# Kernel tuning notes

Hardware: AMD Instinct MI355X
Metric: run time of the kernel (lower is better)

Reference implementation:

```python
import jax, jax.numpy as jnp
import numpy as np

EPS = 1e-5
GN_GROUPS_DIV = 4  # nn.GroupNorm(out_ch // 4, out_ch)


def conv1x1(x, w, b=None):
    # x [B,C,H,W], w [O,C]
    y = jnp.einsum('bchw,oc->bohw', x, w)
    return y if b is None else y + b[None, :, None, None]


def conv2d(x, w, pad):
    return jax.lax.conv_general_dilated(
        x, w, (1, 1), [(pad, pad), (pad, pad)],
        dimension_numbers=('NCHW', 'OIHW', 'NCHW'))


def batchnorm(x, gamma, beta):
    # training-mode BatchNorm2d: batch statistics over (B,H,W)
    mu = jnp.mean(x, axis=(0, 2, 3), keepdims=True)
    var = jnp.var(x, axis=(0, 2, 3), keepdims=True)
    xn = (x - mu) * jax.lax.rsqrt(var + EPS)
    return xn * gamma[None, :, None, None] + beta[None, :, None, None]


def groupnorm(x, gamma, beta, groups):
    B, C, H, W = x.shape
    xg = x.reshape(B, groups, C // groups, H, W)
    mu = jnp.mean(xg, axis=(2, 3, 4), keepdims=True)
    var = jnp.var(xg, axis=(2, 3, 4), keepdims=True)
    xn = ((xg - mu) * jax.lax.rsqrt(var + EPS)).reshape(B, C, H, W)
    return xn * gamma[None, :, None, None] + beta[None, :, None, None]


def bilinear_sample(img, ys, xs):
    # Faithful to DSC._bilinear_interpolate_3D: floor/floor+1 coords are
    # clamped BEFORE computing weights, so samples exactly at the last
    # row/col get all-zero weights (output zeroed there), as in torch.
    H, W = img.shape[2], img.shape[3]
    y0 = jnp.floor(ys)
    x0 = jnp.floor(xs)
    y0c = jnp.clip(y0, 0, H - 1).astype(jnp.int32)
    y1c = jnp.clip(y0 + 1, 0, H - 1).astype(jnp.int32)
    x0c = jnp.clip(x0, 0, W - 1).astype(jnp.int32)
    x1c = jnp.clip(x0 + 1, 0, W - 1).astype(jnp.int32)
    y0f, y1f = y0c.astype(ys.dtype), y1c.astype(ys.dtype)
    x0f, x1f = x0c.astype(xs.dtype), x1c.astype(xs.dtype)
    w00 = (y1f - ys) * (x1f - xs)
    w01 = (y1f - ys) * (xs - x0f)
    w10 = (ys - y0f) * (x1f - xs)
    w11 = (ys - y0f) * (xs - x0f)
    g = lambda yy, xx: img[:, :, yy, xx]  # irregular gather, [B,C,H,W]
    return (g(y0c, x0c) * w00 + g(y0c, x1c) * w01 +
            g(y1c, x0c) * w10 + g(y1c, x1c) * w11)


def _forward(x, ca_w1, ca_w2, sa_w, gate_w, off_w, off_b, off_gamma, off_beta,
             dsc_w, dsc_b, gn_gamma, gn_beta, bn_gamma, bn_beta, prelu_a,
             out_w, out_b):
    B, C, H, W = x.shape
    res = x

    # --- ChannelAttention2D (CBAM): shared MLP on avg & max pooled desc ---
    avg = jnp.mean(x, axis=(2, 3), keepdims=True)          # [B,C,1,1]
    mx = jnp.max(x, axis=(2, 3), keepdims=True)
    mlp = lambda v: conv1x1(jax.nn.relu(conv1x1(v, ca_w1)), ca_w2)
    ca = jax.nn.sigmoid(mlp(avg) + mlp(mx))
    x_ca = x * ca

    # --- SpatialAttention2D (CBAM): 7x7 conv over [mean,max] channel maps ---
    s_avg = jnp.mean(x, axis=1, keepdims=True)
    s_max = jnp.max(x, axis=1, keepdims=True)
    sa = jax.nn.sigmoid(conv2d(jnp.concatenate([s_avg, s_max], axis=1), sa_w, pad=3))
    x_sa = x * sa

    # --- gate fuse ---
    fuse = x_sa + x_ca
    guide = jax.nn.sigmoid(conv1x1(fuse, gate_w))
    xg = x * guide

    # --- DSConv(kernel_size=1, morph=0, if_offset=True) ---
    # offset branch (computed as in torch; with num_points=1 the iterative
    # offset accumulation zeroes the center point, so offsets do NOT move
    # the sampling grid -> zero gradient flows to the offset conv)
    off = jnp.tanh(batchnorm(conv2d(xg, off_w, pad=1) + off_b[None, :, None, None],
                             off_gamma, off_beta))
    del off  # dead in fwd math for kernel_size=1 (faithful to source)

    ii = jnp.arange(H, dtype=x.dtype)[:, None] * jnp.ones((1, W), x.dtype)
    jj = jnp.ones((H, 1), x.dtype) * jnp.arange(W, dtype=x.dtype)[None, :]
    deformed = bilinear_sample(xg, ii, jj)  # identity gather except last row/col zeroed

    d = conv1x1(deformed, dsc_w, dsc_b)     # dsc_conv_x with (k,1)=(1,1) kernel
    d = groupnorm(d, gn_gamma, gn_beta, C // GN_GROUPS_DIV)
    d = jax.nn.relu(d)

    # --- residual + BN + PReLU + 1x1 out conv ---
    y = d + res
    y = batchnorm(y, bn_gamma, bn_beta)
    a = prelu_a.reshape(())
    y = jnp.where(y >= 0, y, a * y)
    return conv1x1(y, out_w, out_b)         # [B,1,H,W]


def setup_inputs() -> dict:
    key = jax.random.key(0)
    ks = jax.random.split(key, 12)
    B, C, H, W = 8, 64, 256, 256
    r = C // 16  # CBAM ratio 16
    f32 = jnp.float32
    n = lambda k, shp, s: (jax.random.normal(k, shp, dtype=f32) * s)
    return {
        'x': n(ks[0], (B, C, H, W), 1.0),
        'ca_w1': n(ks[1], (r, C), 0.1),
        'ca_w2': n(ks[2], (C, r), 0.1),
        'sa_w': n(ks[3], (1, 2, 7, 7), 0.1),
        'gate_w': n(ks[4], (C, C), 0.05),
        'off_w': n(ks[5], (2, C, 3, 3), 0.05),
        'off_b': jnp.zeros((2,), f32),
        'off_gamma': jnp.ones((2,), f32),
        'off_beta': jnp.zeros((2,), f32),
        'dsc_w': n(ks[6], (C, C), 0.05),
        'dsc_b': jnp.zeros((C,), f32),
        'gn_gamma': jnp.ones((C,), f32),
        'gn_beta': jnp.zeros((C,), f32),
        'bn_gamma': jnp.ones((C,), f32),
        'bn_beta': jnp.zeros((C,), f32),
        'prelu_a': jnp.full((1,), 0.25, f32),
        'out_w': n(ks[7], (1, C), 0.1),
        'out_b': jnp.zeros((1,), f32),
    }


def reference(x, ca_w1, ca_w2, sa_w, gate_w, off_w, off_b, off_gamma, off_beta,
              dsc_w, dsc_b, gn_gamma, gn_beta, bn_gamma, bn_beta, prelu_a,
              out_w, out_b):
    return _forward(x, ca_w1, ca_w2, sa_w, gate_w, off_w, off_b, off_gamma,
                    off_beta, dsc_w, dsc_b, gn_gamma, gn_beta, bn_gamma,
                    bn_beta, prelu_a, out_w, out_b)
```

## Files before the change

kernel.cpp:

```cpp
#include <hip/hip_runtime.h>

#define HW 65536
#define CB 64
#define NB 8

typedef __attribute__((ext_vector_type(4))) float f32x4;
typedef __attribute__((ext_vector_type(8))) short s16x8;

__device__ __forceinline__ float sigm(float v) { return 1.f / (1.f + __expf(-v)); }

__device__ __forceinline__ unsigned encf(float f) {
    unsigned u = __float_as_uint(f);
    return (u & 0x80000000u) ? ~u : (u | 0x80000000u);
}
__device__ __forceinline__ float decf(unsigned u) {
    return (u & 0x80000000u) ? __uint_as_float(u & 0x7fffffffu) : __uint_as_float(~u);
}
__device__ __forceinline__ unsigned f2bf(float f) {
    unsigned u = __float_as_uint(f);
    u += 0x7fffu + ((u >> 16) & 1u);
    return u >> 16;
}
__device__ __forceinline__ float bf2f(unsigned h) {
    return __uint_as_float(h << 16);
}
__device__ __forceinline__ int swz(int row, int w) { return (row << 5) + (w ^ ((row & 7) << 2)); }

__global__ __launch_bounds__(256) void k_stats(
    const float* __restrict__ x, float* __restrict__ pool_sum,
    unsigned* __restrict__ pool_max, float* __restrict__ s_avg,
    float* __restrict__ s_max)
{
    const int t = threadIdx.x;
    const int b = blockIdx.x >> 6;
    const int pbase = (blockIdx.x & 63) << 10;
    const int lane = t & 63, wave = t >> 6;
    __shared__ float csum[4][CB];
    __shared__ float cmax[4][CB];

    float ps0 = 0, ps1 = 0, ps2 = 0, ps3 = 0;
    float pm0 = -1e30f, pm1 = -1e30f, pm2 = -1e30f, pm3 = -1e30f;
    const size_t base = (size_t)b * CB * HW + pbase + 4 * t;
    for (int c = 0; c < CB; ++c) {
        const float4 v = *(const float4*)(x + base + (size_t)c * HW);
        ps0 += v.x; ps1 += v.y; ps2 += v.z; ps3 += v.w;
        pm0 = fmaxf(pm0, v.x); pm1 = fmaxf(pm1, v.y);
        pm2 = fmaxf(pm2, v.z); pm3 = fmaxf(pm3, v.w);
        float cs = v.x + v.y + v.z + v.w;
        float cm = fmaxf(fmaxf(v.x, v.y), fmaxf(v.z, v.w));
        #pragma unroll
        for (int off = 32; off; off >>= 1) {
            cs += __shfl_xor(cs, off);
            cm = fmaxf(cm, __shfl_xor(cm, off));
        }
        if (lane == 0) { csum[wave][c] = cs; cmax[wave][c] = cm; }
    }
    __syncthreads();
    if (t < CB) {
        const float s = csum[0][t] + csum[1][t] + csum[2][t] + csum[3][t];
        const float m = fmaxf(fmaxf(cmax[0][t], cmax[1][t]), fmaxf(cmax[2][t], cmax[3][t]));
        atomicAdd(&pool_sum[b * CB + t], s);
        atomicMax(&pool_max[b * CB + t], encf(m));
    }
    const float inv = 1.f / 64.f;
    float4 sa4 = {ps0 * inv, ps1 * inv, ps2 * inv, ps3 * inv};
    float4 sm4 = {pm0, pm1, pm2, pm3};
    *(float4*)(s_avg + (size_t)b * HW + pbase + 4 * t) = sa4;
    *(float4*)(s_max + (size_t)b * HW + pbase + 4 * t) = sm4;
}

__global__ __launch_bounds__(64) void k_ca(
    const float* __restrict__ pool_sum, const unsigned* __restrict__ pool_max,
    const float* __restrict__ w1, const float* __restrict__ w2,
    float* __restrict__ ca)
{
    __shared__ float av[CB], mv[CB], hh[8];
    const int b = blockIdx.x, t = threadIdx.x;
    av[t] = pool_sum[b * CB + t] * (1.f / (float)HW);
    mv[t] = decf(pool_max[b * CB + t]);
    __syncthreads();
    if (t < 8) {
        const int h = t & 3;
        const float* v = (t < 4) ? av : mv;
        float s = 0;
        for (int c = 0; c < CB; ++c) s += w1[h * CB + c] * v[c];
        hh[t] = fmaxf(s, 0.f);
    }
    __syncthreads();
    float s = 0;
    #pragma unroll
    for (int h = 0; h < 4; ++h) s += w2[t * 4 + h] * (hh[h] + hh[4 + h]);
    ca[b * CB + t] = sigm(s);
}

__global__ __launch_bounds__(256) void k_saconv(
    const float* __restrict__ s_avg, const float* __restrict__ s_max,
    const float* __restrict__ w, float* __restrict__ sa)
{
    const int b = blockIdx.x >> 8;
    const int pix = ((blockIdx.x & 255) << 8) | threadIdx.x;
    const int i = pix >> 8, j = pix & 255;
    float acc = 0.f;
    #pragma unroll
    for (int cin = 0; cin < 2; ++cin) {
        const float* src = (cin ? s_max : s_avg) + (size_t)b * HW;
        const float* wk = w + cin * 49;
        #pragma unroll
        for (int ki = 0; ki < 7; ++ki) {
            const int y = i + ki - 3;
            if ((unsigned)y < 256u) {
                #pragma unroll
                for (int kj = 0; kj < 7; ++kj) {
                    const int xx = j + kj - 3;
                    if ((unsigned)xx < 256u) acc += src[(y << 8) | xx] * wk[ki * 7 + kj];
                }
            }
        }
    }
    sa[(size_t)b * HW + pix] = sigm(acc);
}

__global__ __launch_bounds__(256, 3) void k_main(
    const float* __restrict__ x, const float* __restrict__ sa,
    const float* __restrict__ ca, const float* __restrict__ gw,
    const float* __restrict__ dw, const float* __restrict__ db,
    unsigned short* __restrict__ dbuf, float* __restrict__ gn_sum,
    float* __restrict__ gn_sq)
{
    __shared__ unsigned lds[12320];
    const int t = threadIdx.x;
    const int wv = t >> 6, l = t & 63, hi = l >> 4, lo = l & 15;
    const int b = blockIdx.x >> 9;
    const int pbase = (blockIdx.x & 511) << 7;

    {
        const int orow = t >> 2, cq = (t & 3) << 4;
        const float* gsrc = gw + (orow << 6) + cq;
        const float* dsrc = dw + (orow << 6) + cq;
        unsigned ug[8], ud[8];
        #pragma unroll
        for (int j = 0; j < 8; ++j) {
            ug[j] = f2bf(gsrc[2 * j]) | (f2bf(gsrc[2 * j + 1]) << 16);
            ud[j] = f2bf(dsrc[2 * j]) | (f2bf(dsrc[2 * j + 1]) << 16);
        }
        const int wbase = (t & 3) << 3;
        *(uint4*)&lds[swz(orow, wbase)]            = make_uint4(ug[0], ug[1], ug[2], ug[3]);
        *(uint4*)&lds[swz(orow, wbase + 4)]        = make_uint4(ug[4], ug[5], ug[6], ug[7]);
        *(uint4*)&lds[2048 + swz(orow, wbase)]     = make_uint4(ud[0], ud[1], ud[2], ud[3]);
        *(uint4*)&lds[2048 + swz(orow, wbase + 4)] = make_uint4(ud[4], ud[5], ud[6], ud[7]);
    }

    {
        const int px0 = l << 1;
        const float2 sv = *(const float2*)(sa + (size_t)b * HW + pbase + px0);
        unsigned ux0[8], ux1[8], uf0[8], uf1[8];
        #pragma unroll
        for (int j2 = 0; j2 < 8; ++j2) {
            const int c0 = (wv << 4) + 2 * j2;
            const float cv0 = ca[(b << 6) + c0];
            const float cv1 = ca[(b << 6) + c0 + 1];
            const float2 v0 = *(const float2*)(x + ((size_t)((b << 6) + c0)) * HW + pbase + px0);
            const float2 v1 = *(const float2*)(x + ((size_t)((b << 6) + c0 + 1)) * HW + pbase + px0);
            ux0[j2] = f2bf(v0.x) | (f2bf(v1.x) << 16);
            ux1[j2] = f2bf(v0.y) | (f2bf(v1.y) << 16);
            uf0[j2] = f2bf(v0.x * (sv.x + cv0)) | (f2bf(v1.x * (sv.x + cv1)) << 16);
            uf1[j2] = f2bf(v0.y * (sv.y + cv0)) | (f2bf(v1.y * (sv.y + cv1)) << 16);
        }
        const int wb = wv << 3;
        *(uint4*)&lds[8192 + swz(px0, wb)]         = make_uint4(ux0[0], ux0[1], ux0[2], ux0[3]);
        *(uint4*)&lds[8192 + swz(px0, wb + 4)]     = make_uint4(ux0[4], ux0[5], ux0[6], ux0[7]);
        *(uint4*)&lds[8192 + swz(px0 + 1, wb)]     = make_uint4(ux1[0], ux1[1], ux1[2], ux1[3]);
        *(uint4*)&lds[8192 + swz(px0 + 1, wb + 4)] = make_uint4(ux1[4], ux1[5], ux1[6], ux1[7]);
        *(uint4*)&lds[4096 + swz(px0, wb)]         = make_uint4(uf0[0], uf0[1], uf0[2], uf0[3]);
        *(uint4*)&lds[4096 + swz(px0, wb + 4)]     = make_uint4(uf0[4], uf0[5], uf0[6], uf0[7]);
        *(uint4*)&lds[4096 + swz(px0 + 1, wb)]     = make_uint4(uf1[0], uf1[1], uf1[2], uf1[3]);
        *(uint4*)&lds[4096 + swz(px0 + 1, wb + 4)] = make_uint4(uf1[4], uf1[5], uf1[6], uf1[7]);
    }
    __syncthreads();

    f32x4 acc[8];
    #pragma unroll
    for (int n = 0; n < 8; ++n) acc[n] = (f32x4){0.f, 0.f, 0.f, 0.f};
    {
        const int arow = (wv << 4) + lo;
        const s16x8 a0 = __builtin_bit_cast(s16x8, *(const uint4*)&lds[swz(arow, hi << 2)]);
        const s16x8 a1 = __builtin_bit_cast(s16x8, *(const uint4*)&lds[swz(arow, (hi << 2) + 16)]);
        #pragma unroll
        for (int n = 0; n < 8; ++n) {
            const int brow = (n << 4) + lo;
            const s16x8 b0 = __builtin_bit_cast(s16x8, *(const uint4*)&lds[4096 + swz(brow, hi << 2)]);
            const s16x8 b1 = __builtin_bit_cast(s16x8, *(const uint4*)&lds[4096 + swz(brow, (hi << 2) + 16)]);
            acc[n] = __builtin_amdgcn_mfma_f32_16x16x32_bf16(a0, b0, acc[n], 0, 0, 0);
            acc[n] = __builtin_amdgcn_mfma_f32_16x16x32_bf16(a1, b1, acc[n], 0, 0, 0);
        }
    }
    __syncthreads();

    {
        const bool row255 = (pbase >> 8) == 255;
        const bool halfblk = (pbase & 128) != 0;
        const int wb2 = (wv << 3) + (hi << 1);
        #pragma unroll
        for (int n = 0; n < 8; ++n) {
            const int pxl = (n << 4) + lo;
            const uint2 xv = *(const uint2*)&lds[8192 + swz(pxl, wb2)];
            const bool zero = row255 || (halfblk && pxl == 127);
            float xg0 = zero ? 0.f : bf2f(xv.x & 0xffffu) * sigm(acc[n][0]);
            float xg1 = zero ? 0.f : bf2f(xv.x >> 16)     * sigm(acc[n][1]);
            float xg2 = zero ? 0.f : bf2f(xv.y & 0xffffu) * sigm(acc[n][2]);
            float xg3 = zero ? 0.f : bf2f(xv.y >> 16)     * sigm(acc[n][3]);
            uint2 o;
            o.x = f2bf(xg0) | (f2bf(xg1) << 16);
            o.y = f2bf(xg2) | (f2bf(xg3) << 16);
            *(uint2*)&lds[4096 + swz(pxl, wb2)] = o;
        }
    }
    __syncthreads();

    f32x4 acc2[8];
    #pragma unroll
    for (int n = 0; n < 8; ++n) acc2[n] = (f32x4){0.f, 0.f, 0.f, 0.f};
    {
        const int arow = (wv << 4) + lo;
        const s16x8 a0 = __builtin_bit_cast(s16x8, *(const uint4*)&lds[2048 + swz(arow, hi << 2)]);
        const s16x8 a1 = __builtin_bit_cast(s16x8, *(const uint4*)&lds[2048 + swz(arow, (hi << 2) + 16)]);
        #pragma unroll
        for (int n = 0; n < 8; ++n) {
            const int brow = (n << 4) + lo;
            const s16x8 b0 = __builtin_bit_cast(s16x8, *(const uint4*)&lds[4096 + swz(brow, hi << 2)]);
            const s16x8 b1 = __builtin_bit_cast(s16x8, *(const uint4*)&lds[4096 + swz(brow, (hi << 2) + 16)]);
            acc2[n] = __builtin_amdgcn_mfma_f32_16x16x32_bf16(a0, b0, acc2[n], 0, 0, 0);
            acc2[n] = __builtin_amdgcn_mfma_f32_16x16x32_bf16(a1, b1, acc2[n], 0, 0, 0);
        }
    }

    float gs = 0.f, gq = 0.f;
    {
        const float4 bv = *(const float4*)(db + (wv << 4) + (hi << 2));
        const float bvr[4] = {bv.x, bv.y, bv.z, bv.w};
        unsigned short* lds16 = (unsigned short*)lds;
        #pragma unroll
        for (int n = 0; n < 8; ++n) {
            const int pxl = (n << 4) + lo;
            #pragma unroll
            for (int r = 0; r < 4; ++r) {
                const float dvf = acc2[n][r] + bvr[r];
                gs += dvf; gq += dvf * dvf;
                const int ch = (wv << 4) + (hi << 2) + r;
                const int w64 = (pxl >> 1) ^ ((ch & 7) << 2);
                lds16[((8192 + (ch << 6) + w64) << 1) + (pxl & 1)] = (unsigned short)f2bf(dvf);
            }
        }
    }
    #pragma unroll
    for (int o = 1; o < 16; o <<= 1) { gs += __shfl_xor(gs, o); gq += __shfl_xor(gq, o); }
    float* smf = (float*)&lds[12288];
    if (lo == 0) { smf[(((wv << 2) + hi) << 1)] = gs; smf[(((wv << 2) + hi) << 1) + 1] = gq; }
    __syncthreads();
    if (t < 16) {
        atomicAdd(&gn_sum[(b << 4) + t], smf[2 * t]);
        atomicAdd(&gn_sq[(b << 4) + t],  smf[2 * t + 1]);
    }
    {
        const int ch = t >> 2, sub = t & 3;
        unsigned short* dst = dbuf + ((size_t)((b << 6) + ch)) * HW + pbase;
        #pragma unroll
        for (int j = 0; j < 4; ++j) {
            const int w64 = ((j << 4) + (sub << 2)) ^ ((ch & 7) << 2);
            const uint4 dv = *(const uint4*)&lds[8192 + (ch << 6) + w64];
            *(uint4*)(dst + (j << 5) + (sub << 3)) = dv;
        }
    }
}

__global__ void k_fin_gn(const float* __restrict__ gn_sum, const float* __restrict__ gn_sq,
                         const float* __restrict__ gamma, const float* __restrict__ beta,
                         float* __restrict__ gn_a, float* __restrict__ gn_b)
{
    const int t = threadIdx.x;
    const int b = t >> 6, c = t & 63, g = c >> 2;
    const float n = 4.f * (float)HW;
    const float mu = gn_sum[b * 16 + g] / n;
    const float var = gn_sq[b * 16 + g] / n - mu * mu;
    const float a = rsqrtf(var + 1e-5f) * gamma[c];
    gn_a[t] = a;
    gn_b[t] = beta[c] - mu * a;
}

__global__ __launch_bounds__(256) void k_gnbn(
    const float* __restrict__ x, unsigned short* __restrict__ dy,
    const float* __restrict__ gn_a, const float* __restrict__ gn_b,
    float* __restrict__ bn_sum, float* __restrict__ bn_sq)
{
    const int t = threadIdx.x;
    const int bc = blockIdx.x >> 2;
    const int q = blockIdx.x & 3;
    const int c = bc & 63;
    const float a = gn_a[bc], bb = gn_b[bc];
    const size_t base0 = (size_t)bc * HW + ((size_t)q << 14);
    float bs = 0.f, bq = 0.f;
    for (int i = 0; i < 16; ++i) {
        const size_t base = base0 + (i << 10) + (t << 2);
        const ushort4 d4 = *(const ushort4*)(dy + base);
        const float4 xv = *(const float4*)(x + base);
        const float y0 = fmaxf(bf2f(d4.x) * a + bb, 0.f) + xv.x;
        const float y1 = fmaxf(bf2f(d4.y) * a + bb, 0.f) + xv.y;
        const float y2 = fmaxf(bf2f(d4.z) * a + bb, 0.f) + xv.z;
        const float y3 = fmaxf(bf2f(d4.w) * a + bb, 0.f) + xv.w;
        ushort4 o;
        o.x = (unsigned short)f2bf(y0); o.y = (unsigned short)f2bf(y1);
        o.z = (unsigned short)f2bf(y2); o.w = (unsigned short)f2bf(y3);
        *(ushort4*)(dy + base) = o;
        bs += y0 + y1 + y2 + y3;
        bq += y0 * y0 + y1 * y1 + y2 * y2 + y3 * y3;
    }
    #pragma unroll
    for (int off = 32; off; off >>= 1) { bs += __shfl_xor(bs, off); bq += __shfl_xor(bq, off); }
    __shared__ float rs[4], rq[4];
    if ((t & 63) == 0) { rs[t >> 6] = bs; rq[t >> 6] = bq; }
    __syncthreads();
    if (t == 0) {
        atomicAdd(&bn_sum[c], rs[0] + rs[1] + rs[2] + rs[3]);
        atomicAdd(&bn_sq[c],  rq[0] + rq[1] + rq[2] + rq[3]);
    }
}

__global__ void k_fin_bn(const float* __restrict__ bn_sum, const float* __restrict__ bn_sq,
                         const float* __restrict__ gamma, const float* __restrict__ beta,
                         float* __restrict__ bn_a, float* __restrict__ bn_b)
{
    const int c = threadIdx.x;
    const float n = (float)(NB * (size_t)HW);
    const float mu = bn_sum[c] / n;
    const float var = bn_sq[c] / n - mu * mu;
    const float a = rsqrtf(var + 1e-5f) * gamma[c];
    bn_a[c] = a;
    bn_b[c] = beta[c] - mu * a;
}

__global__ __launch_bounds__(256) void k_out(
    const unsigned short* __restrict__ y, const float* __restrict__ bn_a,
    const float* __restrict__ bn_b, const float* __restrict__ pa,
    const float* __restrict__ ow, const float* __restrict__ ob,
    float* __restrict__ out)
{
    const int t = threadIdx.x;
    const int b = blockIdx.x >> 6;
    const int p = ((blockIdx.x & 63) << 10) + (t << 2);
    const float alpha = pa[0];
    const float obv = ob[0];
    float a0 = obv, a1 = obv, a2 = obv, a3 = obv;
    for (int c = 0; c < CB; ++c) {
        const ushort4 v = *(const ushort4*)(y + ((size_t)(b * CB + c)) * HW + p);
        const float s = bn_a[c], sh = bn_b[c], w = ow[c];
        float t0 = bf2f(v.x) * s + sh; t0 = t0 >= 0.f ? t0 : alpha * t0; a0 += w * t0;
        float t1 = bf2f(v.y) * s + sh; t1 = t1 >= 0.f ? t1 : alpha * t1; a1 += w * t1;
        float t2 = bf2f(v.z) * s + sh; t2 = t2 >= 0.f ? t2 : alpha * t2; a2 += w * t2;
        float t3 = bf2f(v.w) * s + sh; t3 = t3 >= 0.f ? t3 : alpha * t3; a3 += w * t3;
    }
    float4 o = {a0, a1, a2, a3};
    *(float4*)(out + (size_t)b * HW + p) = o;
}

extern "C" void kernel_launch(void* const* d_in, const int* in_sizes, int n_in,
                              void* d_out, int out_size, void* d_ws, size_t ws_size,
                              hipStream_t stream)
{
    const float* x        = (const float*)d_in[0];
    const float* ca_w1    = (const float*)d_in[1];
    const float* ca_w2    = (const float*)d_in[2];
    const float* sa_w     = (const float*)d_in[3];
    const float* gate_w   = (const float*)d_in[4];
    const float* dsc_w    = (const float*)d_in[9];
    const float* dsc_b    = (const float*)d_in[10];
    const float* gn_gamma = (const float*)d_in[11];
    const float* gn_beta  = (const float*)d_in[12];
    const float* bn_gamma = (const float*)d_in[13];
    const float* bn_beta  = (const float*)d_in[14];
    const float* prelu_a  = (const float*)d_in[15];
    const float* out_w    = (const float*)d_in[16];
    const float* out_b    = (const float*)d_in[17];
    float* out = (float*)d_out;

    char* ws = (char*)d_ws;
    size_t off = 0;
    auto alloc = [&](size_t bytes) -> char* {
        char* p = ws + off;
        off = (off + bytes + 255) & ~(size_t)255;
        return p;
    };
    unsigned short* dbuf = (unsigned short*)alloc((size_t)NB * CB * HW * 2);
    float* s_avg = (float*)alloc((size_t)NB * HW * 4);
    float* s_max = (float*)alloc((size_t)NB * HW * 4);
    float* sa    = (float*)alloc((size_t)NB * HW * 4);
    float* cav   = (float*)alloc(512 * 4);
    float* gn_a  = (float*)alloc(512 * 4);
    float* gn_b  = (float*)alloc(512 * 4);
    float* bn_a  = (float*)alloc(64 * 4);
    float* bn_b  = (float*)alloc(64 * 4);
    char* stats  = alloc(1408 * 4);
    float*    pool_sum = (float*)stats;
    unsigned* pool_max = (unsigned*)(stats + 512 * 4);
    float*    gn_sum   = (float*)(stats + 1024 * 4);
    float*    gn_sq    = (float*)(stats + 1152 * 4);
    float*    bn_sum   = (float*)(stats + 1280 * 4);
    float*    bn_sq    = (float*)(stats + 1344 * 4);
    (void)in_sizes; (void)n_in; (void)out_size; (void)ws_size;

    hipMemsetAsync(stats, 0, 1408 * 4, stream);

    k_stats <<<NB * 64,      256, 0, stream>>>(x, pool_sum, pool_max, s_avg, s_max);
    k_ca    <<<NB,            64, 0, stream>>>(pool_sum, pool_max, ca_w1, ca_w2, cav);
    k_saconv<<<NB * 256,     256, 0, stream>>>(s_avg, s_max, sa_w, sa);
    k_main  <<<NB * 512,     256, 0, stream>>>(x, sa, cav, gate_w, dsc_w, dsc_b, dbuf, gn_sum, gn_sq);
    k_fin_gn<<<1,            512, 0, stream>>>(gn_sum, gn_sq, gn_gamma, gn_beta, gn_a, gn_b);
    k_gnbn  <<<NB * CB * 4,  256, 0, stream>>>(x, dbuf, gn_a, gn_b, bn_sum, bn_sq);
    k_fin_bn<<<1,             64, 0, stream>>>(bn_sum, bn_sq, bn_gamma, bn_beta, bn_a, bn_b);
    k_out   <<<NB * 64,      256, 0, stream>>>(dbuf, bn_a, bn_b, prelu_a, out_w, out_b, out);
}
```

Before: 193.1 us.

## Switch intermediates to pixel-major bf16 layout and fold finalize kernels into consumers

```diff
diff --git a/kernel.cpp b/kernel.cpp
--- a/kernel.cpp
+++ b/kernel.cpp
@@ -32,73 +32,59 @@
     float* __restrict__ s_max)
 {
     const int t = threadIdx.x;
-    const int b = blockIdx.x >> 6;
-    const int pbase = (blockIdx.x & 63) << 10;
-    const int lane = t & 63, wave = t >> 6;
-    __shared__ float csum[4][CB];
-    __shared__ float cmax[4][CB];
-
-    float ps0 = 0, ps1 = 0, ps2 = 0, ps3 = 0;
-    float pm0 = -1e30f, pm1 = -1e30f, pm2 = -1e30f, pm3 = -1e30f;
+    const int b = blockIdx.x >> 5;
+    const int pbase = (blockIdx.x & 31) << 11;
+    __shared__ float ls[64][65];
+    __shared__ float lm[64][65];
+    float ps[8], pm[8];
+    #pragma unroll
+    for (int i = 0; i < 8; ++i) { ps[i] = 0.f; pm[i] = -1e30f; }
     const size_t base = (size_t)b * CB * HW + pbase + 4 * t;
     for (int c = 0; c < CB; ++c) {
-        const float4 v = *(const float4*)(x + base + (size_t)c * HW);
-        ps0 += v.x; ps1 += v.y; ps2 += v.z; ps3 += v.w;
-        pm0 = fmaxf(pm0, v.x); pm1 = fmaxf(pm1, v.y);
-        pm2 = fmaxf(pm2, v.z); pm3 = fmaxf(pm3, v.w);
-        float cs = v.x + v.y + v.z + v.w;
-        float cm = fmaxf(fmaxf(v.x, v.y), fmaxf(v.z, v.w));
-        #pragma unroll
-        for (int off = 32; off; off >>= 1) {
-            cs += __shfl_xor(cs, off);
-            cm = fmaxf(cm, __shfl_xor(cm, off));
-        }
-        if (lane == 0) { csum[wave][c] = cs; cmax[wave][c] = cm; }
+        const float4 v0 = *(const float4*)(x + base + (size_t)c * HW);
+        const float4 v1 = *(const float4*)(x + base + (size_t)c * HW + 1024);
+        ps[0] += v0.x; ps[1] += v0.y; ps[2] += v0.z; ps[3] += v0.w;
+        ps[4] += v1.x; ps[5] += v1.y; ps[6] += v1.z; ps[7] += v1.w;
+        pm[0] = fmaxf(pm[0], v0.x); pm[1] = fmaxf(pm[1], v0.y);
+        pm[2] = fmaxf(pm[2], v0.z); pm[3] = fmaxf(pm[3], v0.w);
+        pm[4] = fmaxf(pm[4], v1.x); pm[5] = fmaxf(pm[5], v1.y);
+        pm[6] = fmaxf(pm[6], v1.z); pm[7] = fmaxf(pm[7], v1.w);
+        float cs = (v0.x + v0.y + v0.z + v0.w) + (v1.x + v1.y + v1.z + v1.w);
+        float cm = fmaxf(fmaxf(fmaxf(v0.x, v0.y), fmaxf(v0.z, v0.w)),
+                         fmaxf(fmaxf(v1.x, v1.y), fmaxf(v1.z, v1.w)));
+        cs += __shfl_xor(cs, 1); cs += __shfl_xor(cs, 2);
+        cm = fmaxf(cm, __shfl_xor(cm, 1)); cm = fmaxf(cm, __shfl_xor(cm, 2));
+        if ((t & 3) == 0) { ls[c][t >> 2] = cs; lm[c][t >> 2] = cm; }
     }
     __syncthreads();
     if (t < CB) {
-        const float s = csum[0][t] + csum[1][t] + csum[2][t] + csum[3][t];
-        const float m = fmaxf(fmaxf(cmax[0][t], cmax[1][t]), fmaxf(cmax[2][t], cmax[3][t]));
+        float s = 0.f, m = -1e30f;
+        #pragma unroll 8
+        for (int l = 0; l < 64; ++l) { s += ls[t][l]; m = fmaxf(m, lm[t][l]); }
         atomicAdd(&pool_sum[b * CB + t], s);
         atomicMax(&pool_max[b * CB + t], encf(m));
     }
     const float inv = 1.f / 64.f;
-    float4 sa4 = {ps0 * inv, ps1 * inv, ps2 * inv, ps3 * inv};
-    float4 sm4 = {pm0, pm1, pm2, pm3};
-    *(float4*)(s_avg + (size_t)b * HW + pbase + 4 * t) = sa4;
-    *(float4*)(s_max + (size_t)b * HW + pbase + 4 * t) = sm4;
-}
-
-__global__ __launch_bounds__(64) void k_ca(
+    float4 a0 = {ps[0] * inv, ps[1] * inv, ps[2] * inv, ps[3] * inv};
+    float4 a1 = {ps[4] * inv, ps[5] * inv, ps[6] * inv, ps[7] * inv};
+    float4 m0 = {pm[0], pm[1], pm[2], pm[3]};
+    float4 m1 = {pm[4], pm[5], pm[6], pm[7]};
+    *(float4*)(s_avg + (size_t)b * HW + pbase + 4 * t)        = a0;
+    *(float4*)(s_avg + (size_t)b * HW + pbase + 1024 + 4 * t) = a1;
+    *(float4*)(s_max + (size_t)b * HW + pbase + 4 * t)        = m0;
+    *(float4*)(s_max + (size_t)b * HW + pbase + 1024 + 4 * t) = m1;
+}
+
+__global__ __launch_bounds__(256) void k_sa_ca(
+    const float* __restrict__ s_avg, const float* __restrict__ s_max,
+    const float* __restrict__ w,
     const float* __restrict__ pool_sum, const unsigned* __restrict__ pool_max,
     const float* __restrict__ w1, const float* __restrict__ w2,
-    float* __restrict__ ca)
-{
-    __shared__ float av[CB], mv[CB], hh[8];
-    const int b = blockIdx.x, t = threadIdx.x;
-    av[t] = pool_sum[b * CB + t] * (1.f / (float)HW);
-    mv[t] = decf(pool_max[b * CB + t]);
-    __syncthreads();
-    if (t < 8) {
-        const int h = t & 3;
-        const float* v = (t < 4) ? av : mv;
-        float s = 0;
-        for (int c = 0; c < CB; ++c) s += w1[h * CB + c] * v[c];
-        hh[t] = fmaxf(s, 0.f);
-    }
-    __syncthreads();
-    float s = 0;
-    #pragma unroll
-    for (int h = 0; h < 4; ++h) s += w2[t * 4 + h] * (hh[h] + hh[4 + h]);
-    ca[b * CB + t] = sigm(s);
-}
-
-__global__ __launch_bounds__(256) void k_saconv(
-    const float* __restrict__ s_avg, const float* __restrict__ s_max,
-    const float* __restrict__ w, float* __restrict__ sa)
-{
+    float* __restrict__ sa, float* __restrict__ ca)
+{
+    const int t = threadIdx.x;
     const int b = blockIdx.x >> 8;
-    const int pix = ((blockIdx.x & 255) << 8) | threadIdx.x;
+    const int pix = ((blockIdx.x & 255) << 8) | t;
     const int i = pix >> 8, j = pix & 255;
     float acc = 0.f;
     #pragma unroll
@@ -118,14 +104,37 @@
         }
     }
     sa[(size_t)b * HW + pix] = sigm(acc);
+
+    if ((blockIdx.x & 255) == 0) {
+        __shared__ float av[CB], mv[CB], hh[8];
+        if (t < CB) {
+            av[t] = pool_sum[b * CB + t] * (1.f / (float)HW);
+            mv[t] = decf(pool_max[b * CB + t]);
+        }
+        __syncthreads();
+        if (t < 8) {
+            const int h = t & 3;
+            const float* v = (t < 4) ? av : mv;
+            float s = 0;
+            for (int c = 0; c < CB; ++c) s += w1[h * CB + c] * v[c];
+            hh[t] = fmaxf(s, 0.f);
+        }
+        __syncthreads();
+        if (t < CB) {
+            float s = 0;
+            #pragma unroll
+            for (int h = 0; h < 4; ++h) s += w2[t * 4 + h] * (hh[h] + hh[4 + h]);
+            ca[b * CB + t] = sigm(s);
+        }
+    }
 }
 
 __global__ __launch_bounds__(256, 3) void k_main(
     const float* __restrict__ x, const float* __restrict__ sa,
     const float* __restrict__ ca, const float* __restrict__ gw,
     const float* __restrict__ dw, const float* __restrict__ db,
-    unsigned short* __restrict__ dbuf, float* __restrict__ gn_sum,
-    float* __restrict__ gn_sq)
+    unsigned short* __restrict__ dbuf, unsigned short* __restrict__ xpc,
+    float* __restrict__ gn_sum, float* __restrict__ gn_sq)
 {
     __shared__ unsigned lds[12320];
     const int t = threadIdx.x;
@@ -237,19 +246,27 @@
     float gs = 0.f, gq = 0.f;
     {
         const float4 bv = *(const float4*)(db + (wv << 4) + (hi << 2));
-        const float bvr[4] = {bv.x, bv.y, bv.z, bv.w};
-        unsigned short* lds16 = (unsigned short*)lds;
+        unsigned short* dp = dbuf + (((size_t)b * HW + pbase) << 6) + (wv << 4) + (hi << 2);
         #pragma unroll
         for (int n = 0; n < 8; ++n) {
             const int pxl = (n << 4) + lo;
-            #pragma unroll
-            for (int r = 0; r < 4; ++r) {
-                const float dvf = acc2[n][r] + bvr[r];
-                gs += dvf; gq += dvf * dvf;
-                const int ch = (wv << 4) + (hi << 2) + r;
-                const int w64 = (pxl >> 1) ^ ((ch & 7) << 2);
-                lds16[((8192 + (ch << 6) + w64) << 1) + (pxl & 1)] = (unsigned short)f2bf(dvf);
-            }
+            const float d0 = acc2[n][0] + bv.x, d1 = acc2[n][1] + bv.y;
+            const float d2 = acc2[n][2] + bv.z, d3 = acc2[n][3] + bv.w;
+            gs += d0 + d1 + d2 + d3;
+            gq += d0 * d0 + d1 * d1 + d2 * d2 + d3 * d3;
+            uint2 o;
+            o.x = f2bf(d0) | (f2bf(d1) << 16);
+            o.y = f2bf(d2) | (f2bf(d3) << 16);
+            *(uint2*)(dp + ((size_t)pxl << 6)) = o;
+        }
+    }
+    {
+        const int px = t >> 1, hf = t & 1;
+        unsigned short* xp = xpc + (((size_t)b * HW + pbase + px) << 6) + (hf << 5);
+        #pragma unroll
+        for (int q = 0; q < 4; ++q) {
+            const uint4 v = *(const uint4*)&lds[8192 + swz(px, (hf << 4) + (q << 2))];
+            *(uint4*)(xp + (q << 3)) = v;
         }
     }
     #pragma unroll
@@ -261,105 +278,118 @@
         atomicAdd(&gn_sum[(b << 4) + t], smf[2 * t]);
         atomicAdd(&gn_sq[(b << 4) + t],  smf[2 * t + 1]);
     }
-    {
-        const int ch = t >> 2, sub = t & 3;
-        unsigned short* dst = dbuf + ((size_t)((b << 6) + ch)) * HW + pbase;
-        #pragma unroll
-        for (int j = 0; j < 4; ++j) {
-            const int w64 = ((j << 4) + (sub << 2)) ^ ((ch & 7) << 2);
-            const uint4 dv = *(const uint4*)&lds[8192 + (ch << 6) + w64];
-            *(uint4*)(dst + (j << 5) + (sub << 3)) = dv;
-        }
-    }
-}
-
-__global__ void k_fin_gn(const float* __restrict__ gn_sum, const float* __restrict__ gn_sq,
-                         const float* __restrict__ gamma, const float* __restrict__ beta,
-                         float* __restrict__ gn_a, float* __restrict__ gn_b)
+}
+
+__global__ __launch_bounds__(256) void k_gnbn(
+    const unsigned short* __restrict__ xpc, unsigned short* __restrict__ dy,
+    const float* __restrict__ gn_sum, const float* __restrict__ gn_sq,
+    const float* __restrict__ gamma, const float* __restrict__ beta,
+    float* __restrict__ bn_scr)
 {
     const int t = threadIdx.x;
-    const int b = t >> 6, c = t & 63, g = c >> 2;
-    const float n = 4.f * (float)HW;
-    const float mu = gn_sum[b * 16 + g] / n;
-    const float var = gn_sq[b * 16 + g] / n - mu * mu;
-    const float a = rsqrtf(var + 1e-5f) * gamma[c];
-    gn_a[t] = a;
-    gn_b[t] = beta[c] - mu * a;
-}
-
-__global__ __launch_bounds__(256) void k_gnbn(
-    const float* __restrict__ x, unsigned short* __restrict__ dy,
-    const float* __restrict__ gn_a, const float* __restrict__ gn_b,
-    float* __restrict__ bn_sum, float* __restrict__ bn_sq)
+    const size_t P0 = (size_t)blockIdx.x << 8;
+    const int b = (int)(P0 >> 16);
+    __shared__ float ga[CB], gb[CB];
+    __shared__ float red[4][128];
+    if (t < CB) {
+        const int g = t >> 2;
+        const float n4 = 4.f * (float)HW;
+        const float mu = gn_sum[b * 16 + g] / n4;
+        const float var = gn_sq[b * 16 + g] / n4 - mu * mu;
+        const float a = rsqrtf(var + 1e-5f) * gamma[t];
+        ga[t] = a; gb[t] = beta[t] - mu * a;
+    }
+    __syncthreads();
+    const int o8 = (t & 7) << 3;
+    float ar[8], br[8];
+    #pragma unroll
+    for (int k = 0; k < 8; ++k) { ar[k] = ga[o8 + k]; br[k] = gb[o8 + k]; }
+    float as[8], aq[8];
+    #pragma unroll
+    for (int k = 0; k < 8; ++k) { as[k] = 0.f; aq[k] = 0.f; }
+    for (int i = 0; i < 8; ++i) {
+        const size_t P = P0 + (i << 5) + (t >> 3);
+        const size_t idx = (P << 6) + o8;
+        const uint4 dv = *(const uint4*)(dy + idx);
+        const uint4 xv = *(const uint4*)(xpc + idx);
+        const unsigned dw_[4] = {dv.x, dv.y, dv.z, dv.w};
+        const unsigned xw_[4] = {xv.x, xv.y, xv.z, xv.w};
+        uint4 o;
+        unsigned ow_[4];
+        #pragma unroll
+        for (int p = 0; p < 4; ++p) {
+            const int k0 = 2 * p;
+            const float y0 = fmaxf(bf2f(dw_[p] & 0xffffu) * ar[k0] + br[k0], 0.f) + bf2f(xw_[p] & 0xffffu);
+            const float y1 = fmaxf(bf2f(dw_[p] >> 16) * ar[k0 + 1] + br[k0 + 1], 0.f) + bf2f(xw_[p] >> 16);
+            as[k0] += y0; aq[k0] += y0 * y0;
+            as[k0 + 1] += y1; aq[k0 + 1] += y1 * y1;
+            ow_[p] = f2bf(y0) | (f2bf(y1) << 16);
+        }
+        o.x = ow_[0]; o.y = ow_[1]; o.z = ow_[2]; o.w = ow_[3];
+        *(uint4*)(dy + idx) = o;
+    }
+    #pragma unroll
+    for (int k = 0; k < 8; ++k) {
+        #pragma unroll
+        for (int m = 8; m < 64; m <<= 1) {
+            as[k] += __shfl_xor(as[k], m);
+            aq[k] += __shfl_xor(aq[k], m);
+        }
+    }
+    if ((t & 63) < 8) {
+        const int o = t & 7, wvv = t >> 6;
+        #pragma unroll
+        for (int k = 0; k < 8; ++k) {
+            red[wvv][o * 16 + k] = as[k];
+            red[wvv][o * 16 + 8 + k] = aq[k];
+        }
+    }
+    __syncthreads();
+    if (t < 128) {
+        const int o = t >> 4, st = (t >> 3) & 1, k = t & 7;
+        const float v = red[0][t] + red[1][t] + red[2][t] + red[3][t];
+        atomicAdd(&bn_scr[(blockIdx.x & 7) * 128 + st * 64 + o * 8 + k], v);
+    }
+}
+
+__global__ __launch_bounds__(256) void k_out(
+    const unsigned short* __restrict__ y, const float* __restrict__ bn_scr,
+    const float* __restrict__ gamma, const float* __restrict__ beta,
+    const float* __restrict__ pa, const float* __restrict__ ow,
+    const float* __restrict__ ob, float* __restrict__ out)
 {
     const int t = threadIdx.x;
-    const int bc = blockIdx.x >> 2;
-    const int q = blockIdx.x & 3;
-    const int c = bc & 63;
-    const float a = gn_a[bc], bb = gn_b[bc];
-    const size_t base0 = (size_t)bc * HW + ((size_t)q << 14);
-    float bs = 0.f, bq = 0.f;
-    for (int i = 0; i < 16; ++i) {
-        const size_t base = base0 + (i << 10) + (t << 2);
-        const ushort4 d4 = *(const ushort4*)(dy + base);
-        const float4 xv = *(const float4*)(x + base);
-        const float y0 = fmaxf(bf2f(d4.x) * a + bb, 0.f) + xv.x;
-        const float y1 = fmaxf(bf2f(d4.y) * a + bb, 0.f) + xv.y;
-        const float y2 = fmaxf(bf2f(d4.z) * a + bb, 0.f) + xv.z;
-        const float y3 = fmaxf(bf2f(d4.w) * a + bb, 0.f) + xv.w;
-        ushort4 o;
-        o.x = (unsigned short)f2bf(y0); o.y = (unsigned short)f2bf(y1);
-        o.z = (unsigned short)f2bf(y2); o.w = (unsigned short)f2bf(y3);
-        *(ushort4*)(dy + base) = o;
-        bs += y0 + y1 + y2 + y3;
-        bq += y0 * y0 + y1 * y1 + y2 * y2 + y3 * y3;
-    }
-    #pragma unroll
-    for (int off = 32; off; off >>= 1) { bs += __shfl_xor(bs, off); bq += __shfl_xor(bq, off); }
-    __shared__ float rs[4], rq[4];
-    if ((t & 63) == 0) { rs[t >> 6] = bs; rq[t >> 6] = bq; }
-    __syncthreads();
-    if (t == 0) {
-        atomicAdd(&bn_sum[c], rs[0] + rs[1] + rs[2] + rs[3]);
-        atomicAdd(&bn_sq[c],  rq[0] + rq[1] + rq[2] + rq[3]);
-    }
-}
-
-__global__ void k_fin_bn(const float* __restrict__ bn_sum, const float* __restrict__ bn_sq,
-                         const float* __restrict__ gamma, const float* __restrict__ beta,
-                         float* __restrict__ bn_a, float* __restrict__ bn_b)
-{
-    const int c = threadIdx.x;
-    const float n = (float)(NB * (size_t)HW);
-    const float mu = bn_sum[c] / n;
-    const float var = bn_sq[c] / n - mu * mu;
-    const float a = rsqrtf(var + 1e-5f) * gamma[c];
-    bn_a[c] = a;
-    bn_b[c] = beta[c] - mu * a;
-}
-
-__global__ __launch_bounds__(256) void k_out(
-    const unsigned short* __restrict__ y, const float* __restrict__ bn_a,
-    const float* __restrict__ bn_b, const float* __restrict__ pa,
-    const float* __restrict__ ow, const float* __restrict__ ob,
-    float* __restrict__ out)
-{
-    const int t = threadIdx.x;
-    const int b = blockIdx.x >> 6;
-    const int p = ((blockIdx.x & 63) << 10) + (t << 2);
+    __shared__ float A[CB], Bs[CB], W[CB];
+    if (t < CB) {
+        float s = 0.f, q = 0.f;
+        #pragma unroll
+        for (int r = 0; r < 8; ++r) { s += bn_scr[r * 128 + t]; q += bn_scr[r * 128 + 64 + t]; }
+        const float n = (float)NB * (float)HW;
+        const float mu = s / n;
+        const float var = q / n - mu * mu;
+        const float a = rsqrtf(var + 1e-5f) * gamma[t];
+        A[t] = a; Bs[t] = beta[t] - mu * a; W[t] = ow[t];
+    }
+    __syncthreads();
+    const size_t P = ((size_t)blockIdx.x << 8) + t;
+    const unsigned short* yp = y + (P << 6);
     const float alpha = pa[0];
-    const float obv = ob[0];
-    float a0 = obv, a1 = obv, a2 = obv, a3 = obv;
-    for (int c = 0; c < CB; ++c) {
-        const ushort4 v = *(const ushort4*)(y + ((size_t)(b * CB + c)) * HW + p);
-        const float s = bn_a[c], sh = bn_b[c], w = ow[c];
-        float t0 = bf2f(v.x) * s + sh; t0 = t0 >= 0.f ? t0 : alpha * t0; a0 += w * t0;
-        float t1 = bf2f(v.y) * s + sh; t1 = t1 >= 0.f ? t1 : alpha * t1; a1 += w * t1;
-        float t2 = bf2f(v.z) * s + sh; t2 = t2 >= 0.f ? t2 : alpha * t2; a2 += w * t2;
-        float t3 = bf2f(v.w) * s + sh; t3 = t3 >= 0.f ? t3 : alpha * t3; a3 += w * t3;
-    }
-    float4 o = {a0, a1, a2, a3};
-    *(float4*)(out + (size_t)b * HW + p) = o;
+    float acc = ob[0];
+    #pragma unroll
+    for (int q = 0; q < 8; ++q) {
+        const uint4 v = *(const uint4*)(yp + (q << 3));
+        const unsigned vw[4] = {v.x, v.y, v.z, v.w};
+        #pragma unroll
+        for (int p = 0; p < 4; ++p) {
+            const int c = (q << 3) + 2 * p;
+            float z0 = bf2f(vw[p] & 0xffffu) * A[c] + Bs[c];
+            float z1 = bf2f(vw[p] >> 16) * A[c + 1] + Bs[c + 1];
+            z0 = z0 >= 0.f ? z0 : alpha * z0;
+            z1 = z1 >= 0.f ? z1 : alpha * z1;
+            acc += W[c] * z0 + W[c + 1] * z1;
+        }
+    }
+    out[P] = acc;
 }
 
 extern "C" void kernel_launch(void* const* d_in, const int* in_sizes, int n_in,
@@ -389,32 +419,28 @@
         off = (off + bytes + 255) & ~(size_t)255;
         return p;
     };
-    unsigned short* dbuf = (unsigned short*)alloc((size_t)NB * CB * HW * 2);
+    unsigned short* dbuf = (unsigned short*)alloc((size_t)NB * HW * CB * 2);
+    unsigned short* xpc  = (unsigned short*)alloc((size_t)NB * HW * CB * 2);
     float* s_avg = (float*)alloc((size_t)NB * HW * 4);
     float* s_max = (float*)alloc((size_t)NB * HW * 4);
     float* sa    = (float*)alloc((size_t)NB * HW * 4);
     float* cav   = (float*)alloc(512 * 4);
-    float* gn_a  = (float*)alloc(512 * 4);
-    float* gn_b  = (float*)alloc(512 * 4);
-    float* bn_a  = (float*)alloc(64 * 4);
-    float* bn_b  = (float*)alloc(64 * 4);
-    char* stats  = alloc(1408 * 4);
+    char* stats  = alloc(2304 * 4);
     float*    pool_sum = (float*)stats;
     unsigned* pool_max = (unsigned*)(stats + 512 * 4);
     float*    gn_sum   = (float*)(stats + 1024 * 4);
     float*    gn_sq    = (float*)(stats + 1152 * 4);
-    float*    bn_sum   = (float*)(stats + 1280 * 4);
-    float*    bn_sq    = (float*)(stats + 1344 * 4);
+    float*    bn_scr   = (float*)(stats + 1280 * 4);
     (void)in_sizes; (void)n_in; (void)out_size; (void)ws_size;
 
-    hipMemsetAsync(stats, 0, 1408 * 4, stream);
-
-    k_stats <<<NB * 64,      256, 0, stream>>>(x, pool_sum, pool_max, s_avg, s_max);
-    k_ca    <<<NB,            64, 0, stream>>>(pool_sum, pool_max, ca_w1, ca_w2, cav);
-    k_saconv<<<NB * 256,     256, 0, stream>>>(s_avg, s_max, sa_w, sa);
-    k_main  <<<NB * 512,     256, 0, stream>>>(x, sa, cav, gate_w, dsc_w, dsc_b, dbuf, gn_sum, gn_sq);
-    k_fin_gn<<<1,            512, 0, stream>>>(gn_sum, gn_sq, gn_gamma, gn_beta, gn_a, gn_b);
-    k_gnbn  <<<NB * CB * 4,  256, 0, stream>>>(x, dbuf, gn_a, gn_b, bn_sum, bn_sq);
-    k_fin_bn<<<1,             64, 0, stream>>>(bn_sum, bn_sq, bn_gamma, bn_beta, bn_a, bn_b);
-    k_out   <<<NB * 64,      256, 0, stream>>>(dbuf, bn_a, bn_b, prelu_a, out_w, out_b, out);
-}
+    hipMemsetAsync(stats, 0, 2304 * 4, stream);
+
+    k_stats<<<NB * 32,  256, 0, stream>>>(x, pool_sum, pool_max, s_avg, s_max);
+    k_sa_ca<<<NB * 256, 256, 0, stream>>>(s_avg, s_max, sa_w, pool_sum, pool_max,
+                                          ca_w1, ca_w2, sa, cav);
+    k_main <<<NB * 512, 256, 0, stream>>>(x, sa, cav, gate_w, dsc_w, dsc_b,
+                                          dbuf, xpc, gn_sum, gn_sq);
+    k_gnbn <<<2048,     256, 0, stream>>>(xpc, dbuf, gn_sum, gn_sq, gn_gamma, gn_beta, bn_scr);
+    k_out  <<<2048,     256, 0, stream>>>(dbuf, bn_scr, bn_gamma, bn_beta,
+                                          prelu_a, out_w, out_b, out);
+}
```

After: 208.7 us. 1.08x slower.
